# Optimization experiments

Hardware: AMD Instinct MI355X
Metric: run time of the kernel (lower is better)

The kernel has to match this reference:

```python
import jax, jax.numpy as jnp
import numpy as np
from jax import lax

N = 512      # num_nodes in the graph
FEAT = 128   # args.feat_dim (node tag vocab)
EMB = 64     # embedding_size (input_feat width = 2*EMB = 128, per node_order.repeat(1,128))
HID = 128    # args.hidden / LSTM hidden size
NMLP = 4


def setup_inputs() -> dict:
    key = jax.random.key(0)
    ks = jax.random.split(key, 12)
    s = 0.05
    return {
        "node_tags": jax.random.randint(ks[0], (N,), 0, FEAT),
        "adj": jax.random.uniform(ks[1], (N, N), dtype=jnp.float32),
        "label": jax.random.randint(ks[2], (1,), 0, 2),
        "W_emb": jax.random.normal(ks[3], (FEAT, EMB), jnp.float32) * s,
        "b_emb": jnp.zeros((EMB,), jnp.float32),
        "W_ih": jax.random.normal(ks[4], (4 * HID, 2 * EMB), jnp.float32) * s,
        "W_hh": jax.random.normal(ks[5], (4 * HID, HID), jnp.float32) * s,
        "b_ih": jnp.zeros((4 * HID,), jnp.float32),
        "b_hh": jnp.zeros((4 * HID,), jnp.float32),
        "W1s": jax.random.normal(ks[6], (NMLP, HID, HID), jnp.float32) * s,
        "b1s": jnp.zeros((NMLP, HID), jnp.float32),
        "W2s": jax.random.normal(ks[7], (NMLP, HID), jnp.float32) * s,
        "b2s": jnp.zeros((NMLP,), jnp.float32),
        "var_raw": jax.random.normal(ks[8], (NMLP,), jnp.float32) * s,
    }


def _node_orders(adj, key):
    """Greedy noisy random-walk ordering from every start node. [N,N] int32."""
    n = adj.shape[0]
    starts = jnp.arange(n)
    keys = jax.random.split(key, n)

    def one_start(start, k):
        mask0 = jnp.ones((n,), jnp.float32).at[start].set(0.0)

        def step(carry, t):
            cur, mask = carry
            noise = jax.random.uniform(jax.random.fold_in(k, t), (n,),
                                       minval=0.01, maxval=0.1)
            prob = jnp.exp(jnp.take(adj, cur, axis=0) + noise)
            prob = (prob / prob.sum()) * mask  # masked: visited -> 0
            nxt = jnp.argmax(prob)
            return (nxt, mask.at[nxt].set(0.0)), nxt

        _, rest = lax.scan(step, (start, mask0), jnp.arange(n - 1))
        return jnp.concatenate([start[None], rest])

    return jax.vmap(one_start)(starts, keys)


def _lstm(x, W_ih, W_hh, b_ih, b_hh):
    # x: [T, B, In] -> out [T, B, H]
    T, B, _ = x.shape
    H = W_hh.shape[1]
    b = b_ih + b_hh

    def step(carry, xt):
        h, c = carry
        gates = xt @ W_ih.T + h @ W_hh.T + b           # [B, 4H]
        i, f, g, o = jnp.split(gates, 4, axis=-1)      # torch gate order i,f,g,o
        c = jax.nn.sigmoid(f) * c + jax.nn.sigmoid(i) * jnp.tanh(g)
        h = jax.nn.sigmoid(o) * jnp.tanh(c)
        return (h, c), h

    h0 = jnp.zeros((B, H), x.dtype)
    _, out = lax.scan(step, (h0, h0), x)
    return out


def reference(node_tags, adj, label, W_emb, b_emb, W_ih, W_hh, b_ih, b_hh,
              W1s, b1s, W2s, b2s, var_raw):
    n = adj.shape[0]
    onehot = jax.nn.one_hot(node_tags, W_emb.shape[0], dtype=jnp.float32)
    node_feat = onehot @ W_emb + b_emb                       # [N, EMB]
    A = (adj > 0.5).astype(jnp.float32)                      # binary adjacency
    neigh_feat = (A @ onehot) @ W_emb + b_emb                # neighbor tag histogram -> embed
    input_feat = jnp.concatenate([node_feat, neigh_feat], 1) # [N, 2*EMB]

    orders = _node_orders(adj, jax.random.key(42))           # [Nstart, Nstep]
    batch = input_feat[orders]                               # [Nstart, Nstep, 2E]
    batch = jnp.transpose(batch, (1, 0, 2))                  # [T=N, B=N, 2E]

    out = _lstm(batch, W_ih, W_hh, b_ih, b_hh)               # [T, B, HID]
    embed = out.mean(axis=0)                                 # [N, HID]

    # 4-way ensemble MLP heads (batched over k)
    h = jax.nn.relu(jnp.einsum('nd,kdh->knh', embed, W1s) + b1s[:, None, :])
    logits = jnp.einsum('knh,kh->kn', h, W2s) + b2s[:, None] # [4, N]
    y = jax.nn.sigmoid(logits)
    lab = label[0].astype(jnp.float32)
    bce = -(lab * jax.nn.log_sigmoid(logits)
            + (1.0 - lab) * jax.nn.log_sigmoid(-logits)).mean(axis=1)  # [4]
    loss_ = bce.sum()

    var_w = jax.nn.softplus(var_raw)                         # per-head weight
    c = var_w / var_w.sum()
    y_ = (c[:, None] * y).sum(axis=0)                        # [N]
    return loss_, y_
```

## Files before the change

kernel.cpp:

```cpp
#include <hip/hip_runtime.h>
#include <hip/hip_bf16.h>
#include <stdint.h>

#define NN 512
#define EMBD 64
#define HID 128

typedef float f32x4 __attribute__((ext_vector_type(4)));
typedef short s16x8 __attribute__((ext_vector_type(8)));

__device__ __forceinline__ uint32_t rotl32(uint32_t v, int s){ return (v << s) | (v >> (32 - s)); }

__device__ __forceinline__ void tf2x32(uint32_t k0, uint32_t k1, uint32_t x0, uint32_t x1,
                                       uint32_t &o0, uint32_t &o1){
  uint32_t k2 = k0 ^ k1 ^ 0x1BD11BDAu;
  x0 += k0; x1 += k1;
  x0+=x1; x1=rotl32(x1,13); x1^=x0;
  x0+=x1; x1=rotl32(x1,15); x1^=x0;
  x0+=x1; x1=rotl32(x1,26); x1^=x0;
  x0+=x1; x1=rotl32(x1, 6); x1^=x0;
  x0 += k1; x1 += k2 + 1u;
  x0+=x1; x1=rotl32(x1,17); x1^=x0;
  x0+=x1; x1=rotl32(x1,29); x1^=x0;
  x0+=x1; x1=rotl32(x1,16); x1^=x0;
  x0+=x1; x1=rotl32(x1,24); x1^=x0;
  x0 += k2; x1 += k0 + 2u;
  x0+=x1; x1=rotl32(x1,13); x1^=x0;
  x0+=x1; x1=rotl32(x1,15); x1^=x0;
  x0+=x1; x1=rotl32(x1,26); x1^=x0;
  x0+=x1; x1=rotl32(x1, 6); x1^=x0;
  x0 += k0; x1 += k1 + 3u;
  x0+=x1; x1=rotl32(x1,17); x1^=x0;
  x0+=x1; x1=rotl32(x1,29); x1^=x0;
  x0+=x1; x1=rotl32(x1,16); x1^=x0;
  x0+=x1; x1=rotl32(x1,24); x1^=x0;
  x0 += k1; x1 += k2 + 4u;
  x0+=x1; x1=rotl32(x1,13); x1^=x0;
  x0+=x1; x1=rotl32(x1,15); x1^=x0;
  x0+=x1; x1=rotl32(x1,26); x1^=x0;
  x0+=x1; x1=rotl32(x1, 6); x1^=x0;
  x0 += k2; x1 += k0 + 5u;
  o0 = x0; o1 = x1;
}

__device__ __forceinline__ float bits_to_noise(uint32_t bits){
  float u = __builtin_bit_cast(float, (bits >> 9) | 0x3f800000u) - 1.0f;
  const float dlt = 0.1f - 0.01f;
  float v = __fadd_rn(__fmul_rn(u, dlt), 0.01f);
  return fmaxf(0.01f, v);
}

__device__ __forceinline__ short f2bf(float f){
  uint32_t u = __builtin_bit_cast(uint32_t, f);
  u += 0x7fffu + ((u >> 16) & 1u);
  return (short)(u >> 16);
}

__device__ __forceinline__ float fsig(float x){
  return __builtin_amdgcn_rcpf(1.0f + __expf(-x));
}
__device__ __forceinline__ float ftanh(float x){
  float e = __expf(2.0f * x);
  return 1.0f - 2.0f * __builtin_amdgcn_rcpf(e + 1.0f);
}
__device__ __forceinline__ float softplusf(float x){
  return log1pf(expf(x));
}

__device__ __forceinline__ float wave_fmax(float x){
  int xi;
  #define DSTEP(C) xi = __builtin_amdgcn_update_dpp(0, __builtin_bit_cast(int,x), C, 0xF, 0xF, true); \
                   x = fmaxf(x, __builtin_bit_cast(float,xi));
  DSTEP(0xB1)
  DSTEP(0x4E)
  DSTEP(0x141)
  DSTEP(0x140)
  #undef DSTEP
  xi = __builtin_amdgcn_ds_swizzle(__builtin_bit_cast(int,x), 0x401F);
  x = fmaxf(x, __builtin_bit_cast(float,xi));
  x = fmaxf(x, __shfl_xor(x, 32));
  return x;
}
__device__ __forceinline__ uint32_t wave_maxu(uint32_t x){
  int m;
  #define USTEP(C) m = __builtin_amdgcn_update_dpp(0, (int)x, C, 0xF, 0xF, true); \
                   x = x > (uint32_t)m ? x : (uint32_t)m;
  USTEP(0xB1) USTEP(0x4E) USTEP(0x141) USTEP(0x140)
  #undef USTEP
  m = __builtin_amdgcn_ds_swizzle((int)x, 0x401F);
  x = x > (uint32_t)m ? x : (uint32_t)m;
  uint32_t o = (uint32_t)__shfl_xor((int)x, 32);
  x = x > o ? x : o;
  return x;
}

__device__ __forceinline__ void orders_body(const float* __restrict__ adj,
                                            int* __restrict__ orders, int s){
  int lane = threadIdx.x;
  __shared__ uint32_t kts[2*(NN-1)];
  __shared__ float ca[NN];
  __shared__ int   ci[NN];

  uint32_t ks0, ks1; tf2x32(0u, 42u, 0u, (uint32_t)s, ks0, ks1);
  for (int t = lane; t < NN-1; t += 64){
    uint32_t a, b; tf2x32(ks0, ks1, 0u, (uint32_t)t, a, b);
    kts[2*t] = a; kts[2*t+1] = b;
  }
  __syncthreads();

  uint32_t vis = 0;
  if ((s >> 3) == lane) vis |= 1u << (s & 7);
  int cur = s;
  if (lane == 0) orders[(size_t)s*NN] = s;
  unsigned long long lt = (1ull << lane) - 1ull;

  for (int t = 0; t < NN-1; ++t){
    uint32_t kt0 = kts[2*t], kt1 = kts[2*t+1];
    const float4* r4 = (const float4*)(adj + (size_t)cur*NN);
    float4 v0 = r4[lane*2], v1 = r4[lane*2+1];
    float a[8] = {v0.x,v0.y,v0.z,v0.w,v1.x,v1.y,v1.z,v1.w};

    float mx = -1.f;
    #pragma unroll
    for (int e = 0; e < 8; ++e)
      mx = fmaxf(mx, ((vis >> e) & 1) ? -1.f : a[e]);
    mx = wave_fmax(mx);
    float T = mx - 0.0901f;

    int base = 0, pos[8]; uint32_t cm = 0;
    #pragma unroll
    for (int e = 0; e < 8; ++e){
      bool c = !((vis >> e) & 1) && (a[e] >= T);
      unsigned long long bal = __ballot(c);
      pos[e] = base + __popcll(bal & lt);
      base += __popcll(bal);
      if (c) cm |= 1u << e;
    }
    #pragma unroll
    for (int e = 0; e < 8; ++e)
      if ((cm >> e) & 1){ ca[pos[e]] = a[e]; ci[pos[e]] = lane*8 + e; }
    int total = base;

    uint32_t bk = 0; int bi = 0x7fffffff;
    for (int b0 = 0; b0 < total; b0 += 64){
      int k = b0 + lane;
      if (k < total){
        int idx = ci[k]; float av = ca[k];
        uint32_t x0, x1;
        tf2x32(kt0, kt1, 0u, (uint32_t)idx, x0, x1);
        float nz = bits_to_noise(x0 ^ x1);
        uint32_t a23 = (uint32_t)(av * 8388608.0f);
        uint32_t n30 = (uint32_t)(nz * 1073741824.0f);
        uint32_t key = (a23 << 7) + n30;
        if (key > bk || (key == bk && idx < bi)){ bk = key; bi = idx; }
      }
    }
    uint32_t km = wave_maxu(bk);
    unsigned long long msk = __ballot(bk == km);
    int widx;
    if (__popcll(msk) == 1){
      widx = __shfl(bi, __ffsll((long long)msk) - 1);
    } else {
      int iv = (bk == km) ? bi : 0x7fffffff;
      #pragma unroll
      for (int off = 1; off < 64; off <<= 1){
        int o = __shfl_xor(iv, off);
        iv = o < iv ? o : iv;
      }
      widx = iv;
    }
    cur = widx;
    if ((widx >> 3) == lane) vis |= 1u << (widx & 7);
    if (lane == 0) orders[(size_t)s*NN + t + 1] = widx;
  }
}

__device__ __forceinline__ void featifw_body(int n, const int* __restrict__ tags,
    const float* __restrict__ adj, const float* __restrict__ W_emb,
    const float* __restrict__ b_emb, const float* __restrict__ W_ih,
    const float* __restrict__ b_ih, const float* __restrict__ b_hh,
    float* __restrict__ IFW){
  int tid = threadIdx.x;
  __shared__ int tg[NN];
  __shared__ __align__(16) float xs[2*EMBD];
  for (int i = tid; i < NN; i += 64) tg[i] = tags[i];
  float nf = W_emb[tg[n]*EMBD + tid] + b_emb[tid];
  float ac = 0.f;
  for (int m = 0; m < NN; ++m){
    if (adj[(size_t)n*NN + m] > 0.5f) ac += W_emb[tg[m]*EMBD + tid];
  }
  xs[tid]        = nf;
  xs[EMBD + tid] = ac + b_emb[tid];
  __syncthreads();
  const float4* xs4 = (const float4*)xs;
  for (int it = 0; it < 8; ++it){
    int g = it*64 + tid;
    const float4* wr4 = (const float4*)(W_ih + (size_t)g*(2*EMBD));
    float acc = b_ih[g] + b_hh[g];
    #pragma unroll 8
    for (int kk = 0; kk < 32; ++kk){
      float4 wv = wr4[kk], xv = xs4[kk];
      acc += wv.x*xv.x + wv.y*xv.y + wv.z*xv.z + wv.w*xv.w;
    }
    IFW[(size_t)n*(4*HID) + g] = acc;
  }
}

__global__ __launch_bounds__(64) void k_mega1(const float* __restrict__ adj,
    int* __restrict__ orders, const int* __restrict__ tags,
    const float* __restrict__ W_emb, const float* __restrict__ b_emb,
    const float* __restrict__ W_ih, const float* __restrict__ b_ih,
    const float* __restrict__ b_hh, float* __restrict__ IFW){
  if (blockIdx.x < NN) orders_body(adj, orders, blockIdx.x);
  else                 featifw_body(blockIdx.x - NN, tags, adj, W_emb, b_emb,
                                    W_ih, b_ih, b_hh, IFW);
}

__device__ __forceinline__ void lstm_step(int t, int w, int l15, int l4,
    const short (*hread)[HID+8], short (*hwrite)[HID+8],
    float (&vIFc)[4][4], float (&vIFn)[4][4],
    const s16x8 (&Bf)[4][4], float (&c)[4], float (&emb)[4],
    const int* ord_s, const float* __restrict__ IFW){
  int tn = (t + 1 < NN) ? t + 1 : NN - 1;
  #pragma unroll
  for (int r = 0; r < 4; ++r){
    int ord = ord_s[(l4*4 + r)*NN + tn];
    const float* base = IFW + (size_t)ord*(4*HID) + w*16 + l15;
    #pragma unroll
    for (int q = 0; q < 4; ++q) vIFn[q][r] = base[q*HID];
  }
  s16x8 Af[4];
  #pragma unroll
  for (int kt = 0; kt < 4; ++kt)
    Af[kt] = *(const s16x8*)&hread[l15][kt*32 + l4*8];
  f32x4 acc[4];
  #pragma unroll
  for (int q = 0; q < 4; ++q){
    f32x4 a = {vIFc[q][0], vIFc[q][1], vIFc[q][2], vIFc[q][3]};
    #pragma unroll
    for (int kt = 0; kt < 4; ++kt)
      a = __builtin_amdgcn_mfma_f32_16x16x32_bf16(Af[kt], Bf[q][kt], a, 0, 0, 0);
    acc[q] = a;
  }
  int col = w*16 + l15;
  #pragma unroll
  for (int r = 0; r < 4; ++r){
    float si = fsig(acc[0][r]);
    float sf = fsig(acc[1][r]);
    float tg = ftanh(acc[2][r]);
    float so = fsig(acc[3][r]);
    float cn = sf * c[r] + si * tg;
    c[r] = cn;
    float h = so * ftanh(cn);
    emb[r] += h;
    hwrite[l4*4 + r][col] = f2bf(h);
  }
  __syncthreads();
}

__global__ __launch_bounds__(512, 2) void k_lstm(const float* __restrict__ W_hh,
    const float* __restrict__ IFW, const int* __restrict__ orders,
    const float* __restrict__ W1s, const float* __restrict__ b1s,
    const float* __restrict__ W2s, const float* __restrict__ b2s,
    float* __restrict__ logits){
  int wg = blockIdx.x, tid = threadIdx.x;
  int w = tid >> 6, l = tid & 63, l15 = l & 15, l4 = l >> 4;
  __shared__ int ord_s[16*NN];
  __shared__ __align__(16) short hbuf[2][16][HID+8];
  __shared__ float part[4][2];

  for (int i = tid; i < 16*NN; i += 512){
    int m = i >> 9, t = i & (NN-1);
    ord_s[i] = orders[(size_t)(16*wg + m)*NN + t];
  }
  for (int i = tid; i < 16*(HID+8); i += 512)
    ((short*)hbuf[0])[i] = 0;

  s16x8 Bf[4][4];
  #pragma unroll
  for (int q = 0; q < 4; ++q)
    #pragma unroll
    for (int kt = 0; kt < 4; ++kt){
      int g = q*HID + w*16 + l15;
      const float* src = W_hh + (size_t)g*HID + kt*32 + l4*8;
      s16x8 v;
      #pragma unroll
      for (int e = 0; e < 8; ++e) v[e] = f2bf(src[e]);
      Bf[q][kt] = v;
    }
  __syncthreads();

  float c[4] = {0,0,0,0}, emb[4] = {0,0,0,0};
  float vA[4][4], vB[4][4];
  #pragma unroll
  for (int r = 0; r < 4; ++r){
    int ord = ord_s[(l4*4 + r)*NN];
    const float* base = IFW + (size_t)ord*(4*HID) + w*16 + l15;
    #pragma unroll
    for (int q = 0; q < 4; ++q) vA[q][r] = base[q*HID];
  }

  for (int t2 = 0; t2 < NN/2; ++t2){
    lstm_step(2*t2,     w, l15, l4, hbuf[0], hbuf[1], vA, vB, Bf, c, emb, ord_s, IFW);
    lstm_step(2*t2 + 1, w, l15, l4, hbuf[1], hbuf[0], vB, vA, Bf, c, emb, ord_s, IFW);
  }

  float* eL = (float*)&hbuf[0][0][0];
  #pragma unroll
  for (int r = 0; r < 4; ++r)
    eL[(l4*4 + r)*HID + w*16 + l15] = emb[r] * (1.0f/512.0f);
  __syncthreads();

  int hk = tid >> 7;
  int u  = tid & 127;
  float b1v = b1s[hk*HID + u];
  float w2v = W2s[hk*HID + u];
  const float* wcol = W1s + (size_t)hk*HID*HID + u;
  for (int m = 0; m < 16; ++m){
    const float4* es4 = (const float4*)(eL + m*HID);
    float pre = b1v;
    #pragma unroll 4
    for (int d4 = 0; d4 < 32; ++d4){
      float4 e4 = es4[d4];
      pre += e4.x * wcol[(4*d4+0)*HID];
      pre += e4.y * wcol[(4*d4+1)*HID];
      pre += e4.z * wcol[(4*d4+2)*HID];
      pre += e4.w * wcol[(4*d4+3)*HID];
    }
    float v = fmaxf(pre, 0.f) * w2v;
    #pragma unroll
    for (int off = 1; off < 64; off <<= 1) v += __shfl_xor(v, off);
    if (l == 0) part[hk][(tid >> 6) & 1] = v;
    __syncthreads();
    if (tid < 4) logits[tid*NN + 16*wg + m] = part[tid][0] + part[tid][1] + b2s[tid];
    __syncthreads();
  }
}

__global__ __launch_bounds__(512) void k_final(const float* __restrict__ logits,
                                               const int* __restrict__ label,
                                               const float* __restrict__ var_raw,
                                               float* __restrict__ out){
  int n = threadIdx.x;
  float lab = (float)label[0];
  float sp[4]; float tot = 0.f;
  #pragma unroll
  for (int k = 0; k < 4; ++k){ sp[k] = softplusf(var_raw[k]); tot += sp[k]; }
  float y = 0.f, bce = 0.f;
  #pragma unroll
  for (int k = 0; k < 4; ++k){
    float x = logits[k*NN + n];
    float yk = 1.0f / (1.0f + expf(-x));
    y += (sp[k] / tot) * yk;
    bce += lab * softplusf(-x) + (1.0f - lab) * softplusf(x);
  }
  out[1 + n] = y;
  __shared__ float pr[8];
  #pragma unroll
  for (int off = 1; off < 64; off <<= 1) bce += __shfl_xor(bce, off);
  if ((n & 63) == 0) pr[n >> 6] = bce;
  __syncthreads();
  if (n == 0){
    float ssum = 0.f;
    for (int i = 0; i < 8; ++i) ssum += pr[i];
    out[0] = ssum * (1.0f/512.0f);
  }
}

extern "C" void kernel_launch(void* const* d_in, const int* in_sizes, int n_in,
                              void* d_out, int out_size, void* d_ws, size_t ws_size,
                              hipStream_t stream) {
  const int*   node_tags = (const int*)  d_in[0];
  const float* adj       = (const float*)d_in[1];
  const int*   label     = (const int*)  d_in[2];
  const float* W_emb     = (const float*)d_in[3];
  const float* b_emb     = (const float*)d_in[4];
  const float* W_ih      = (const float*)d_in[5];
  const float* W_hh      = (const float*)d_in[6];
  const float* b_ih      = (const float*)d_in[7];
  const float* b_hh      = (const float*)d_in[8];
  const float* W1s       = (const float*)d_in[9];
  const float* b1s       = (const float*)d_in[10];
  const float* W2s       = (const float*)d_in[11];
  const float* b2s       = (const float*)d_in[12];
  const float* var_raw   = (const float*)d_in[13];
  float* out = (float*)d_out;

  float* ws     = (float*)d_ws;
  float* IFW    = ws + 65536;
  float* logits = IFW + 262144 + 65536;
  int*   orders = (int*)(logits + 2048);

  k_mega1<<<dim3(2*NN), dim3(64),  0, stream>>>(adj, orders, node_tags, W_emb,
                                                b_emb, W_ih, b_ih, b_hh, IFW);
  k_lstm <<<dim3(32),   dim3(512), 0, stream>>>(W_hh, IFW, orders, W1s, b1s,
                                                W2s, b2s, logits);
  k_final<<<dim3(1),    dim3(512), 0, stream>>>(logits, label, var_raw, out);
}
```

Baseline: 1.127 ms.

## Interleave four random walks per wave and prefetch next adjacency row

The orders stage now runs four independent greedy walks in one 64-thread block, interleaving their steps so the latency of each walk's serial chain can be hidden behind the others. The next row of adj is loaded at the end of each step instead of the start. Separately, the neighbor embedding is rebuilt as a tag histogram built with shared-memory atomics, followed by a 128-term dot with W_emb, replacing a 512-iteration loop of branchy gathers. The cost is four times the shared memory and registers per block and a quarter as many walk blocks, which lowers parallelism across CUs.

```diff
diff --git a/kernel.cpp b/kernel.cpp
--- a/kernel.cpp
+++ b/kernel.cpp
@@ -3,8 +3,10 @@
 #include <stdint.h>
 
 #define NN 512
+#define FEAT 128
 #define EMBD 64
 #define HID 128
+#define WPB 4
 
 typedef float f32x4 __attribute__((ext_vector_type(4)));
 typedef short s16x8 __attribute__((ext_vector_type(8)));
@@ -94,84 +96,106 @@
   return x;
 }
 
-__device__ __forceinline__ void orders_body(const float* __restrict__ adj,
-                                            int* __restrict__ orders, int s){
+__device__ __forceinline__ void walk_step(int t, int lane,
+    const float* __restrict__ adj, int* __restrict__ orders, int s,
+    uint32_t &vis, int &cur, float4 &r0, float4 &r1,
+    const uint32_t* kts, float* ca, int* ci, unsigned long long lt){
+  uint32_t kt0 = kts[2*t], kt1 = kts[2*t+1];
+  float a[8] = {r0.x,r0.y,r0.z,r0.w,r1.x,r1.y,r1.z,r1.w};
+
+  float mx = -1.f;
+  #pragma unroll
+  for (int e = 0; e < 8; ++e)
+    mx = fmaxf(mx, ((vis >> e) & 1) ? -1.f : a[e]);
+  mx = wave_fmax(mx);
+  float T = mx - 0.0901f;
+
+  int base = 0, pos[8]; uint32_t cm = 0;
+  #pragma unroll
+  for (int e = 0; e < 8; ++e){
+    bool c = !((vis >> e) & 1) && (a[e] >= T);
+    unsigned long long bal = __ballot(c);
+    pos[e] = base + __popcll(bal & lt);
+    base += __popcll(bal);
+    if (c) cm |= 1u << e;
+  }
+  #pragma unroll
+  for (int e = 0; e < 8; ++e)
+    if ((cm >> e) & 1){ ca[pos[e]] = a[e]; ci[pos[e]] = lane*8 + e; }
+  int total = base;
+
+  uint32_t bk = 0; int bi = 0x7fffffff;
+  for (int b0 = 0; b0 < total; b0 += 64){
+    int k = b0 + lane;
+    if (k < total){
+      int idx = ci[k]; float av = ca[k];
+      uint32_t x0, x1;
+      tf2x32(kt0, kt1, 0u, (uint32_t)idx, x0, x1);
+      float nz = bits_to_noise(x0 ^ x1);
+      uint32_t a23 = (uint32_t)(av * 8388608.0f);
+      uint32_t n30 = (uint32_t)(nz * 1073741824.0f);
+      uint32_t key = (a23 << 7) + n30;
+      if (key > bk || (key == bk && idx < bi)){ bk = key; bi = idx; }
+    }
+  }
+  uint32_t km = wave_maxu(bk);
+  unsigned long long msk = __ballot(bk == km);
+  int widx;
+  if (__popcll(msk) == 1){
+    widx = __shfl(bi, __ffsll((long long)msk) - 1);
+  } else {
+    int iv = (bk == km) ? bi : 0x7fffffff;
+    #pragma unroll
+    for (int off = 1; off < 64; off <<= 1){
+      int o = __shfl_xor(iv, off);
+      iv = o < iv ? o : iv;
+    }
+    widx = iv;
+  }
+  cur = widx;
+  const float4* nr = (const float4*)(adj + (size_t)widx*NN);
+  r0 = nr[lane*2]; r1 = nr[lane*2+1];
+  if ((widx >> 3) == lane) vis |= 1u << (widx & 7);
+  if (lane == 0) orders[(size_t)s*NN + t + 1] = widx;
+}
+
+__device__ __forceinline__ void orders_quad(const float* __restrict__ adj,
+                                            int* __restrict__ orders, int bid){
   int lane = threadIdx.x;
-  __shared__ uint32_t kts[2*(NN-1)];
-  __shared__ float ca[NN];
-  __shared__ int   ci[NN];
-
-  uint32_t ks0, ks1; tf2x32(0u, 42u, 0u, (uint32_t)s, ks0, ks1);
+  __shared__ uint32_t kts[WPB][2*(NN-1)];
+  __shared__ float ca[WPB][NN];
+  __shared__ int   ci[WPB][NN];
+  int s0 = bid*WPB;
+
+  uint32_t ks[WPB][2];
+  #pragma unroll
+  for (int w = 0; w < WPB; ++w)
+    tf2x32(0u, 42u, 0u, (uint32_t)(s0+w), ks[w][0], ks[w][1]);
   for (int t = lane; t < NN-1; t += 64){
-    uint32_t a, b; tf2x32(ks0, ks1, 0u, (uint32_t)t, a, b);
-    kts[2*t] = a; kts[2*t+1] = b;
-  }
-  __syncthreads();
-
-  uint32_t vis = 0;
-  if ((s >> 3) == lane) vis |= 1u << (s & 7);
-  int cur = s;
-  if (lane == 0) orders[(size_t)s*NN] = s;
+    #pragma unroll
+    for (int w = 0; w < WPB; ++w){
+      uint32_t a, b; tf2x32(ks[w][0], ks[w][1], 0u, (uint32_t)t, a, b);
+      kts[w][2*t] = a; kts[w][2*t+1] = b;
+    }
+  }
+
+  uint32_t vis[WPB]; int cur[WPB]; float4 r0[WPB], r1[WPB];
   unsigned long long lt = (1ull << lane) - 1ull;
+  #pragma unroll
+  for (int w = 0; w < WPB; ++w){
+    int s = s0 + w;
+    vis[w] = ((s >> 3) == lane) ? (1u << (s & 7)) : 0u;
+    cur[w] = s;
+    if (lane == 0) orders[(size_t)s*NN] = s;
+    const float4* r4 = (const float4*)(adj + (size_t)s*NN);
+    r0[w] = r4[lane*2]; r1[w] = r4[lane*2+1];
+  }
 
   for (int t = 0; t < NN-1; ++t){
-    uint32_t kt0 = kts[2*t], kt1 = kts[2*t+1];
-    const float4* r4 = (const float4*)(adj + (size_t)cur*NN);
-    float4 v0 = r4[lane*2], v1 = r4[lane*2+1];
-    float a[8] = {v0.x,v0.y,v0.z,v0.w,v1.x,v1.y,v1.z,v1.w};
-
-    float mx = -1.f;
-    #pragma unroll
-    for (int e = 0; e < 8; ++e)
-      mx = fmaxf(mx, ((vis >> e) & 1) ? -1.f : a[e]);
-    mx = wave_fmax(mx);
-    float T = mx - 0.0901f;
-
-    int base = 0, pos[8]; uint32_t cm = 0;
-    #pragma unroll
-    for (int e = 0; e < 8; ++e){
-      bool c = !((vis >> e) & 1) && (a[e] >= T);
-      unsigned long long bal = __ballot(c);
-      pos[e] = base + __popcll(bal & lt);
-      base += __popcll(bal);
-      if (c) cm |= 1u << e;
-    }
-    #pragma unroll
-    for (int e = 0; e < 8; ++e)
-      if ((cm >> e) & 1){ ca[pos[e]] = a[e]; ci[pos[e]] = lane*8 + e; }
-    int total = base;
-
-    uint32_t bk = 0; int bi = 0x7fffffff;
-    for (int b0 = 0; b0 < total; b0 += 64){
-      int k = b0 + lane;
-      if (k < total){
-        int idx = ci[k]; float av = ca[k];
-        uint32_t x0, x1;
-        tf2x32(kt0, kt1, 0u, (uint32_t)idx, x0, x1);
-        float nz = bits_to_noise(x0 ^ x1);
-        uint32_t a23 = (uint32_t)(av * 8388608.0f);
-        uint32_t n30 = (uint32_t)(nz * 1073741824.0f);
-        uint32_t key = (a23 << 7) + n30;
-        if (key > bk || (key == bk && idx < bi)){ bk = key; bi = idx; }
-      }
-    }
-    uint32_t km = wave_maxu(bk);
-    unsigned long long msk = __ballot(bk == km);
-    int widx;
-    if (__popcll(msk) == 1){
-      widx = __shfl(bi, __ffsll((long long)msk) - 1);
-    } else {
-      int iv = (bk == km) ? bi : 0x7fffffff;
-      #pragma unroll
-      for (int off = 1; off < 64; off <<= 1){
-        int o = __shfl_xor(iv, off);
-        iv = o < iv ? o : iv;
-      }
-      widx = iv;
-    }
-    cur = widx;
-    if ((widx >> 3) == lane) vis |= 1u << (widx & 7);
-    if (lane == 0) orders[(size_t)s*NN + t + 1] = widx;
+    #pragma unroll
+    for (int w = 0; w < WPB; ++w)
+      walk_step(t, lane, adj, orders, s0+w, vis[w], cur[w], r0[w], r1[w],
+                kts[w], ca[w], ci[w], lt);
   }
 }
 
@@ -182,27 +206,36 @@
     float* __restrict__ IFW){
   int tid = threadIdx.x;
   __shared__ int tg[NN];
+  __shared__ float cnt[FEAT];
   __shared__ __align__(16) float xs[2*EMBD];
   for (int i = tid; i < NN; i += 64) tg[i] = tags[i];
-  float nf = W_emb[tg[n]*EMBD + tid] + b_emb[tid];
-  float ac = 0.f;
-  for (int m = 0; m < NN; ++m){
-    if (adj[(size_t)n*NN + m] > 0.5f) ac += W_emb[tg[m]*EMBD + tid];
-  }
-  xs[tid]        = nf;
-  xs[EMBD + tid] = ac + b_emb[tid];
+  cnt[tid] = 0.f; cnt[tid + 64] = 0.f;
+  __syncthreads();
+  const float* row = adj + (size_t)n*NN;
+  #pragma unroll
+  for (int c = 0; c < 8; ++c){
+    float v = row[c*64 + tid];
+    if (v > 0.5f) atomicAdd(&cnt[tg[c*64 + tid]], 1.0f);
+  }
+  __syncthreads();
+  float acc = 0.f;
+  #pragma unroll 16
+  for (int k = 0; k < FEAT; ++k)
+    acc = fmaf(cnt[k], W_emb[k*EMBD + tid], acc);
+  xs[tid]        = W_emb[tg[n]*EMBD + tid] + b_emb[tid];
+  xs[EMBD + tid] = acc + b_emb[tid];
   __syncthreads();
   const float4* xs4 = (const float4*)xs;
   for (int it = 0; it < 8; ++it){
     int g = it*64 + tid;
     const float4* wr4 = (const float4*)(W_ih + (size_t)g*(2*EMBD));
-    float acc = b_ih[g] + b_hh[g];
+    float a2 = b_ih[g] + b_hh[g];
     #pragma unroll 8
     for (int kk = 0; kk < 32; ++kk){
       float4 wv = wr4[kk], xv = xs4[kk];
-      acc += wv.x*xv.x + wv.y*xv.y + wv.z*xv.z + wv.w*xv.w;
-    }
-    IFW[(size_t)n*(4*HID) + g] = acc;
+      a2 += wv.x*xv.x + wv.y*xv.y + wv.z*xv.z + wv.w*xv.w;
+    }
+    IFW[(size_t)n*(4*HID) + g] = a2;
   }
 }
 
@@ -211,9 +244,9 @@
     const float* __restrict__ W_emb, const float* __restrict__ b_emb,
     const float* __restrict__ W_ih, const float* __restrict__ b_ih,
     const float* __restrict__ b_hh, float* __restrict__ IFW){
-  if (blockIdx.x < NN) orders_body(adj, orders, blockIdx.x);
-  else                 featifw_body(blockIdx.x - NN, tags, adj, W_emb, b_emb,
-                                    W_ih, b_ih, b_hh, IFW);
+  if (blockIdx.x < NN/WPB) orders_quad(adj, orders, blockIdx.x);
+  else                     featifw_body(blockIdx.x - NN/WPB, tags, adj, W_emb,
+                                        b_emb, W_ih, b_ih, b_hh, IFW);
 }
 
 __device__ __forceinline__ void lstm_step(int t, int w, int l15, int l4,
@@ -391,9 +424,10 @@
   float* logits = IFW + 262144 + 65536;
   int*   orders = (int*)(logits + 2048);
 
-  k_mega1<<<dim3(2*NN), dim3(64),  0, stream>>>(adj, orders, node_tags, W_emb,
-                                                b_emb, W_ih, b_ih, b_hh, IFW);
-  k_lstm <<<dim3(32),   dim3(512), 0, stream>>>(W_hh, IFW, orders, W1s, b1s,
-                                                W2s, b2s, logits);
-  k_final<<<dim3(1),    dim3(512), 0, stream>>>(logits, label, var_raw, out);
-}
+  k_mega1<<<dim3(NN/WPB + NN), dim3(64), 0, stream>>>(adj, orders, node_tags,
+                                                      W_emb, b_emb, W_ih, b_ih,
+                                                      b_hh, IFW);
+  k_lstm <<<dim3(32),  dim3(512), 0, stream>>>(W_hh, IFW, orders, W1s, b1s,
+                                               W2s, b2s, logits);
+  k_final<<<dim3(1),   dim3(512), 0, stream>>>(logits, label, var_raw, out);
+}
```

Result: slower. 2.577 ms (+128.5%).
